# Performance work log

Hardware: AMD Instinct MI355X
Metric: run time of the kernel (lower is better)

## Reference

```python
import jax, jax.numpy as jnp
import numpy as np

N_NODES = 100000
N_EDGES = 1600000
FEAT = 128
BATCH = 2


def setup_inputs() -> dict:
    key = jax.random.key(0)
    ks = jax.random.split(key, 8)
    scale = 1.0 / np.sqrt(FEAT)
    return {
        "mesh_node_features": jax.random.normal(ks[0], (BATCH, N_NODES, FEAT), jnp.float32),
        "edge_index": jax.random.randint(ks[1], (N_EDGES, 2), 0, N_NODES, jnp.int64),
        "W1": jax.random.normal(ks[2], (FEAT, FEAT), jnp.float32) * scale,
        "b1": jnp.zeros((FEAT,), jnp.float32),
        "W2": jax.random.normal(ks[3], (FEAT, FEAT), jnp.float32) * scale,
        "b2": jnp.zeros((FEAT,), jnp.float32),
        "W3": jax.random.normal(ks[4], (FEAT, FEAT), jnp.float32) * scale,
        "b3": jnp.zeros((FEAT,), jnp.float32),
    }


def _gcn_layer(x, src, dst, norm, W, b, n_nodes):
    # x: [B, N, Fin] -> [B, N, Fout]; GCNConv: project, normalized scatter-sum, bias
    h = jnp.einsum("bnf,fg->bng", x, W)
    msg = h[:, src, :] * norm[None, :, None]          # [B, E+N, Fout]
    out = jnp.zeros_like(h).at[:, dst, :].add(msg)    # scatter over dst nodes
    return out + b


def reference(mesh_node_features, edge_index, W1, b1, W2, b2, W3, b3):
    n = mesh_node_features.shape[1]
    loops = jnp.arange(n, dtype=edge_index.dtype)
    src = jnp.concatenate([edge_index[:, 0], loops])  # self-loops appended
    dst = jnp.concatenate([edge_index[:, 1], loops])
    deg = jnp.zeros((n,), jnp.float32).at[dst].add(1.0)
    dinv = jax.lax.rsqrt(deg)                         # deg >= 1 due to self-loops
    norm = dinv[src] * dinv[dst]                      # symmetric GCN normalization

    x = mesh_node_features
    for W, b in ((W1, b1), (W2, b2), (W3, b3)):
        x = jax.nn.relu(_gcn_layer(x, src, dst, norm, W, b, n))
    return x
```

## Files before the change

### kernel.cpp

```cpp
#include <hip/hip_runtime.h>
#include <hip/hip_bf16.h>
#include <hip/hip_fp16.h>

#ifndef MINi
#define MINi(a,b) ((a)<(b)?(a):(b))
#endif

typedef _Float16 f16x8 __attribute__((ext_vector_type(8)));
typedef _Float16 f16x4 __attribute__((ext_vector_type(4)));
typedef float    f32x4 __attribute__((ext_vector_type(4)));

__global__ __launch_bounds__(256)
void cvt_kernel(const float* __restrict__ in, _Float16* __restrict__ out, int n4)
{
    int i = blockIdx.x * 256 + threadIdx.x;
    if (i >= n4) return;
    float4 v = ((const float4*)in)[i];
    f16x4 st = {(_Float16)v.x, (_Float16)v.y, (_Float16)v.z, (_Float16)v.w};
    ((f16x4*)out)[i] = st;
}

__global__ __launch_bounds__(256)
void wt_kernel(const float* __restrict__ W, _Float16* __restrict__ Wt)
{
    int idx = blockIdx.x * 256 + threadIdx.x;
    int k = idx >> 7, col = idx & 127;
    Wt[col * 128 + k] = (_Float16)W[idx];
}

__global__ __launch_bounds__(256)
void deg_kernel(const int* __restrict__ ei, int* __restrict__ cnt, int nE)
{
    int e = blockIdx.x * 256 + threadIdx.x;
    if (e >= nE) return;
    int2 p = ((const int2*)ei)[e];
    atomicAdd(&cnt[p.y], 1);
}

__global__ __launch_bounds__(256)
void scan_partials(const int* __restrict__ cnt, int* __restrict__ bsum, int n)
{
    __shared__ int red[4];
    int base = blockIdx.x * 1024;
    int t = threadIdx.x;
    int s = 0;
    #pragma unroll
    for (int i = 0; i < 4; ++i) {
        int idx = base + t * 4 + i;
        if (idx < n) s += cnt[idx];
    }
    #pragma unroll
    for (int off = 1; off < 64; off <<= 1) s += __shfl_xor(s, off);
    if ((t & 63) == 0) red[t >> 6] = s;
    __syncthreads();
    if (t == 0) bsum[blockIdx.x] = red[0] + red[1] + red[2] + red[3];
}

__global__ __launch_bounds__(128)
void scan_bsums(int* __restrict__ bsum, int nb)
{
    __shared__ int lds[128];
    int t = threadIdx.x;
    int v = (t < nb) ? bsum[t] : 0;
    lds[t] = v;
    __syncthreads();
    for (int off = 1; off < 128; off <<= 1) {
        int add = (t >= off) ? lds[t - off] : 0;
        __syncthreads();
        lds[t] += add;
        __syncthreads();
    }
    if (t < nb) bsum[t] = lds[t] - v;
}

__global__ __launch_bounds__(256)
void scan_final(const int* __restrict__ cnt, const int* __restrict__ bsum,
                int* __restrict__ row_start, int* __restrict__ cursor,
                float* __restrict__ dinv, int n, int nE)
{
    __shared__ int tsum[256];
    int base = blockIdx.x * 1024;
    int t = threadIdx.x;
    int c[4]; int s = 0;
    #pragma unroll
    for (int i = 0; i < 4; ++i) {
        int idx = base + t * 4 + i;
        c[i] = (idx < n) ? cnt[idx] : 0;
        s += c[i];
    }
    tsum[t] = s;
    __syncthreads();
    for (int off = 1; off < 256; off <<= 1) {
        int add = (t >= off) ? tsum[t - off] : 0;
        __syncthreads();
        tsum[t] += add;
        __syncthreads();
    }
    int run = bsum[blockIdx.x] + tsum[t] - s;
    #pragma unroll
    for (int i = 0; i < 4; ++i) {
        int idx = base + t * 4 + i;
        if (idx < n) {
            row_start[idx] = run;
            cursor[idx]    = run;
            dinv[idx]      = rsqrtf((float)(c[i] + 1));
            run += c[i];
        }
    }
    if (blockIdx.x == 0 && t == 0) row_start[n] = nE;
}

__global__ __launch_bounds__(256)
void fill_kernel(const int* __restrict__ ei, const float* __restrict__ dinv,
                 int* __restrict__ cursor, int2* __restrict__ csr, int nE)
{
    int e = blockIdx.x * 256 + threadIdx.x;
    if (e >= nE) return;
    int2 p = ((const int2*)ei)[e];
    int pos = atomicAdd(&cursor[p.y], 1);
    float nw = dinv[p.x] * dinv[p.y];
    csr[pos] = make_int2(p.x, __float_as_int(nw));
}

__global__ __launch_bounds__(256)
void agg_kernel(const _Float16* __restrict__ x, _Float16* __restrict__ out,
                const int* __restrict__ row_start, const int2* __restrict__ csr,
                const float* __restrict__ dinv, int n)
{
    int d = (blockIdx.x << 2) + (threadIdx.x >> 6);
    if (d >= n) return;
    int lane = threadIdx.x & 63;
    int hb   = lane >> 5;
    int fo   = (lane & 31) << 2;
    const _Float16* xb = x + (size_t)hb * n * 128 + fo;

    float sd = dinv[d], s2 = sd * sd;
    f16x4 xs = *(const f16x4*)(xb + (size_t)d * 128);
    float a0 = s2 * (float)xs[0], a1 = s2 * (float)xs[1];
    float a2 = s2 * (float)xs[2], a3 = s2 * (float)xs[3];

    int rs = row_start[d], re = row_start[d + 1];
    for (int e = rs; e < re; e += 64) {
        int idx = e + lane;
        int2 pk = csr[idx < re ? idx : re - 1];
        int cnt = MINi(re - e, 64);
        #pragma unroll 4
        for (int i = 0; i < cnt; ++i) {
            int   src = __shfl(pk.x, i);
            float nw  = __shfl(__int_as_float(pk.y), i);
            f16x4 rv = *(const f16x4*)(xb + (size_t)src * 128);
            a0 += nw * (float)rv[0]; a1 += nw * (float)rv[1];
            a2 += nw * (float)rv[2]; a3 += nw * (float)rv[3];
        }
    }
    f16x4 st = {(_Float16)a0, (_Float16)a1, (_Float16)a2, (_Float16)a3};
    *(f16x4*)(out + (size_t)(hb * n + d) * 128 + fo) = st;
}

template<bool HALF_OUT>
__global__ __launch_bounds__(256)
void gemm_mfma(const _Float16* __restrict__ A, const _Float16* __restrict__ Wt,
               const float* __restrict__ bias, void* __restrict__ outp, int nrows)
{
    int t  = threadIdx.x;
    int wv = t >> 6;
    int l  = t & 63;
    int lr = l & 15;
    int lk = l >> 4;
    size_t r0 = (size_t)blockIdx.x * 64;
    int c0 = wv * 32;

    f16x8 bf[2][4];
    #pragma unroll
    for (int ct = 0; ct < 2; ++ct)
        #pragma unroll
        for (int ks = 0; ks < 4; ++ks)
            bf[ct][ks] = *(const f16x8*)(Wt + (c0 + ct * 16 + lr) * 128 + ks * 32 + lk * 8);

    f32x4 acc[4][2];
    #pragma unroll
    for (int rt = 0; rt < 4; ++rt) {
        acc[rt][0] = (f32x4){0.f, 0.f, 0.f, 0.f};
        acc[rt][1] = (f32x4){0.f, 0.f, 0.f, 0.f};
    }

    #pragma unroll
    for (int rt = 0; rt < 4; ++rt) {
        #pragma unroll
        for (int ks = 0; ks < 4; ++ks) {
            f16x8 af = *(const f16x8*)(A + (r0 + rt * 16 + lr) * 128 + ks * 32 + lk * 8);
            acc[rt][0] = __builtin_amdgcn_mfma_f32_16x16x32_f16(af, bf[0][ks], acc[rt][0], 0, 0, 0);
            acc[rt][1] = __builtin_amdgcn_mfma_f32_16x16x32_f16(af, bf[1][ks], acc[rt][1], 0, 0, 0);
        }
    }

    float bc0 = bias[c0 + lr];
    float bc1 = bias[c0 + 16 + lr];
    #pragma unroll
    for (int rt = 0; rt < 4; ++rt) {
        #pragma unroll
        for (int ct = 0; ct < 2; ++ct) {
            float bc = ct ? bc1 : bc0;
            int col = c0 + ct * 16 + lr;
            #pragma unroll
            for (int r = 0; r < 4; ++r) {
                float v = fmaxf(acc[rt][ct][r] + bc, 0.f);
                size_t row = r0 + rt * 16 + lk * 4 + r;
                if constexpr (HALF_OUT)
                    ((_Float16*)outp)[row * 128 + col] = (_Float16)v;
                else
                    ((float*)outp)[row * 128 + col] = v;
            }
        }
    }
}

static inline size_t align_up(size_t x, size_t a) { return (x + a - 1) & ~(a - 1); }

extern "C" void kernel_launch(void* const* d_in, const int* in_sizes, int n_in,
                              void* d_out, int out_size, void* d_ws, size_t ws_size,
                              hipStream_t stream)
{
    const float* xin = (const float*)d_in[0];
    const int*   ei  = (const int*)d_in[1];
    const float* W1  = (const float*)d_in[2];
    const float* b1  = (const float*)d_in[3];
    const float* W2  = (const float*)d_in[4];
    const float* b2  = (const float*)d_in[5];
    const float* W3  = (const float*)d_in[6];
    const float* b3  = (const float*)d_in[7];
    float* out = (float*)d_out;

    const int N = in_sizes[0] / 256;
    const int E = in_sizes[1] / 2;
    const int ROWS = 2 * N;

    char* ws = (char*)d_ws;
    size_t off = 0;
    _Float16* Xh = (_Float16*)(ws + off);   off = align_up(off + (size_t)ROWS * 128 * 2, 256);
    _Float16* Ah = (_Float16*)(ws + off);   off = align_up(off + (size_t)ROWS * 128 * 2, 256);
    _Float16* Wt1 = (_Float16*)(ws + off);  off = align_up(off + 16384 * 2, 256);
    _Float16* Wt2 = (_Float16*)(ws + off);  off = align_up(off + 16384 * 2, 256);
    _Float16* Wt3 = (_Float16*)(ws + off);  off = align_up(off + 16384 * 2, 256);
    int* cnt = (int*)(ws + off);            off = align_up(off + (size_t)N * 4, 256);
    int* row_start = (int*)(ws + off);      off = align_up(off + (size_t)(N + 1) * 4, 256);
    int* cursor = (int*)(ws + off);         off = align_up(off + (size_t)N * 4, 256);
    float* dinvp = (float*)(ws + off);      off = align_up(off + (size_t)N * 4, 256);
    int* bsum = (int*)(ws + off);           off = align_up(off + 1024 * 4, 256);
    int2* csr = (int2*)(ws + off);          off = align_up(off + (size_t)E * 8, 256);

    const int nb = (N + 1023) / 1024;

    const int n4 = ROWS * 32;
    cvt_kernel<<<(n4 + 255) / 256, 256, 0, stream>>>(xin, Xh, n4);
    wt_kernel<<<64, 256, 0, stream>>>(W1, Wt1);
    wt_kernel<<<64, 256, 0, stream>>>(W2, Wt2);
    wt_kernel<<<64, 256, 0, stream>>>(W3, Wt3);

    hipMemsetAsync(cnt, 0, (size_t)N * 4, stream);
    deg_kernel<<<(E + 255) / 256, 256, 0, stream>>>(ei, cnt, E);
    scan_partials<<<nb, 256, 0, stream>>>(cnt, bsum, N);
    scan_bsums<<<1, 128, 0, stream>>>(bsum, nb);
    scan_final<<<nb, 256, 0, stream>>>(cnt, bsum, row_start, cursor, dinvp, N, E);
    fill_kernel<<<(E + 255) / 256, 256, 0, stream>>>(ei, dinvp, cursor, csr, E);

    const int agrid = (N + 3) / 4;
    const int ggrid = ROWS / 64;

    agg_kernel<<<agrid, 256, 0, stream>>>(Xh, Ah, row_start, csr, dinvp, N);
    gemm_mfma<true><<<ggrid, 256, 0, stream>>>(Ah, Wt1, b1, Xh, ROWS);
    agg_kernel<<<agrid, 256, 0, stream>>>(Xh, Ah, row_start, csr, dinvp, N);
    gemm_mfma<true><<<ggrid, 256, 0, stream>>>(Ah, Wt2, b2, Xh, ROWS);
    agg_kernel<<<agrid, 256, 0, stream>>>(Xh, Ah, row_start, csr, dinvp, N);
    gemm_mfma<false><<<ggrid, 256, 0, stream>>>(Ah, Wt3, b3, out, ROWS);
}
```

Measured before the change: 860.3 us.

## Fuse aggregation with MFMA GEMM per layer and single-pass decoupled scan

```diff
diff --git a/kernel.cpp b/kernel.cpp
--- a/kernel.cpp
+++ b/kernel.cpp
@@ -11,21 +11,34 @@
 typedef float    f32x4 __attribute__((ext_vector_type(4)));
 
 __global__ __launch_bounds__(256)
-void cvt_kernel(const float* __restrict__ in, _Float16* __restrict__ out, int n4)
-{
-    int i = blockIdx.x * 256 + threadIdx.x;
-    if (i >= n4) return;
-    float4 v = ((const float4*)in)[i];
-    f16x4 st = {(_Float16)v.x, (_Float16)v.y, (_Float16)v.z, (_Float16)v.w};
-    ((f16x4*)out)[i] = st;
-}
-
-__global__ __launch_bounds__(256)
-void wt_kernel(const float* __restrict__ W, _Float16* __restrict__ Wt)
-{
-    int idx = blockIdx.x * 256 + threadIdx.x;
-    int k = idx >> 7, col = idx & 127;
-    Wt[col * 128 + k] = (_Float16)W[idx];
+void prep_kernel(const float* __restrict__ xin, _Float16* __restrict__ Xh,
+                 const float* __restrict__ W1, const float* __restrict__ W2,
+                 const float* __restrict__ W3,
+                 _Float16* __restrict__ Wt1, _Float16* __restrict__ Wt2,
+                 _Float16* __restrict__ Wt3,
+                 int* __restrict__ zbase, int n4, int ncvt, int nzero)
+{
+    int b = blockIdx.x;
+    int t = threadIdx.x;
+    if (b < ncvt) {
+        int i = b * 256 + t;
+        if (i < n4) {
+            float4 v = ((const float4*)xin)[i];
+            f16x4 st = {(_Float16)v.x, (_Float16)v.y, (_Float16)v.z, (_Float16)v.w};
+            ((f16x4*)Xh)[i] = st;
+        }
+    } else if (b < ncvt + 192) {
+        int wb = b - ncvt;
+        int wi = wb >> 6;
+        int idx = (wb & 63) * 256 + t;
+        const float* W = (wi == 0) ? W1 : (wi == 1) ? W2 : W3;
+        _Float16* Wt = (wi == 0) ? Wt1 : (wi == 1) ? Wt2 : Wt3;
+        int k = idx >> 7, col = idx & 127;
+        Wt[col * 128 + k] = (_Float16)W[idx];
+    } else {
+        int i = (b - ncvt - 192) * 256 + t;
+        if (i < nzero) zbase[i] = 0;
+    }
 }
 
 __global__ __launch_bounds__(256)
@@ -37,50 +50,21 @@
     atomicAdd(&cnt[p.y], 1);
 }
 
-__global__ __launch_bounds__(256)
-void scan_partials(const int* __restrict__ cnt, int* __restrict__ bsum, int n)
-{
-    __shared__ int red[4];
-    int base = blockIdx.x * 1024;
+#define FLAG_AGG (1u << 30)
+#define FLAG_INC (2u << 30)
+#define VAL_MASK 0x3FFFFFFFu
+
+__global__ __launch_bounds__(256)
+void scan_kernel(const int* __restrict__ cnt, int* __restrict__ row_start,
+                 int* __restrict__ cursor, float* __restrict__ dinv,
+                 unsigned* __restrict__ status, int n, int nE)
+{
+    __shared__ int tsum[256];
+    __shared__ int sbase;
+    int b = blockIdx.x;
     int t = threadIdx.x;
-    int s = 0;
-    #pragma unroll
-    for (int i = 0; i < 4; ++i) {
-        int idx = base + t * 4 + i;
-        if (idx < n) s += cnt[idx];
-    }
-    #pragma unroll
-    for (int off = 1; off < 64; off <<= 1) s += __shfl_xor(s, off);
-    if ((t & 63) == 0) red[t >> 6] = s;
-    __syncthreads();
-    if (t == 0) bsum[blockIdx.x] = red[0] + red[1] + red[2] + red[3];
-}
-
-__global__ __launch_bounds__(128)
-void scan_bsums(int* __restrict__ bsum, int nb)
-{
-    __shared__ int lds[128];
-    int t = threadIdx.x;
-    int v = (t < nb) ? bsum[t] : 0;
-    lds[t] = v;
-    __syncthreads();
-    for (int off = 1; off < 128; off <<= 1) {
-        int add = (t >= off) ? lds[t - off] : 0;
-        __syncthreads();
-        lds[t] += add;
-        __syncthreads();
-    }
-    if (t < nb) bsum[t] = lds[t] - v;
-}
-
-__global__ __launch_bounds__(256)
-void scan_final(const int* __restrict__ cnt, const int* __restrict__ bsum,
-                int* __restrict__ row_start, int* __restrict__ cursor,
-                float* __restrict__ dinv, int n, int nE)
-{
-    __shared__ int tsum[256];
-    int base = blockIdx.x * 1024;
-    int t = threadIdx.x;
+    int base = b * 1024;
+
     int c[4]; int s = 0;
     #pragma unroll
     for (int i = 0; i < 4; ++i) {
@@ -96,7 +80,35 @@
         tsum[t] += add;
         __syncthreads();
     }
-    int run = bsum[blockIdx.x] + tsum[t] - s;
+
+    if (t == 0) {
+        int total = tsum[255];
+        if (b == 0) {
+            __hip_atomic_store(&status[0], FLAG_INC | (unsigned)total,
+                               __ATOMIC_RELAXED, __HIP_MEMORY_SCOPE_AGENT);
+            sbase = 0;
+        } else {
+            __hip_atomic_store(&status[b], FLAG_AGG | (unsigned)total,
+                               __ATOMIC_RELAXED, __HIP_MEMORY_SCOPE_AGENT);
+            int run = 0;
+            int j = b - 1;
+            while (true) {
+                unsigned w = __hip_atomic_load(&status[j], __ATOMIC_RELAXED,
+                                               __HIP_MEMORY_SCOPE_AGENT);
+                if (w == 0u) { __builtin_amdgcn_s_sleep(1); continue; }
+                run += (int)(w & VAL_MASK);
+                if (w & FLAG_INC) break;
+                --j;
+            }
+            int inc = run + total;
+            __hip_atomic_store(&status[b], FLAG_INC | (unsigned)inc,
+                               __ATOMIC_RELAXED, __HIP_MEMORY_SCOPE_AGENT);
+            sbase = inc - total;
+        }
+    }
+    __syncthreads();
+
+    int run = sbase + tsum[t] - s;
     #pragma unroll
     for (int i = 0; i < 4; ++i) {
         int idx = base + t * 4 + i;
@@ -107,7 +119,7 @@
             run += c[i];
         }
     }
-    if (blockIdx.x == 0 && t == 0) row_start[n] = nE;
+    if (b == 0 && t == 0) row_start[n] = nE;
 }
 
 __global__ __launch_bounds__(256)
@@ -122,95 +134,82 @@
     csr[pos] = make_int2(p.x, __float_as_int(nw));
 }
 
-__global__ __launch_bounds__(256)
-void agg_kernel(const _Float16* __restrict__ x, _Float16* __restrict__ out,
-                const int* __restrict__ row_start, const int2* __restrict__ csr,
-                const float* __restrict__ dinv, int n)
-{
-    int d = (blockIdx.x << 2) + (threadIdx.x >> 6);
-    if (d >= n) return;
-    int lane = threadIdx.x & 63;
+template<bool HALF_OUT>
+__global__ __launch_bounds__(256)
+void fused_kernel(const _Float16* __restrict__ x, void* __restrict__ outp,
+                  const _Float16* __restrict__ Wt, const float* __restrict__ bias,
+                  const int* __restrict__ row_start, const int2* __restrict__ csr,
+                  const float* __restrict__ dinv, int n)
+{
+    __shared__ _Float16 al[64][136];
+    int t    = threadIdx.x;
+    int wv   = t >> 6;
+    int lane = t & 63;
     int hb   = lane >> 5;
     int fo   = (lane & 31) << 2;
+    int d0   = blockIdx.x << 5;
     const _Float16* xb = x + (size_t)hb * n * 128 + fo;
 
-    float sd = dinv[d], s2 = sd * sd;
-    f16x4 xs = *(const f16x4*)(xb + (size_t)d * 128);
-    float a0 = s2 * (float)xs[0], a1 = s2 * (float)xs[1];
-    float a2 = s2 * (float)xs[2], a3 = s2 * (float)xs[3];
-
-    int rs = row_start[d], re = row_start[d + 1];
-    for (int e = rs; e < re; e += 64) {
-        int idx = e + lane;
-        int2 pk = csr[idx < re ? idx : re - 1];
-        int cnt = MINi(re - e, 64);
-        #pragma unroll 4
-        for (int i = 0; i < cnt; ++i) {
-            int   src = __shfl(pk.x, i);
-            float nw  = __shfl(__int_as_float(pk.y), i);
-            f16x4 rv = *(const f16x4*)(xb + (size_t)src * 128);
-            a0 += nw * (float)rv[0]; a1 += nw * (float)rv[1];
-            a2 += nw * (float)rv[2]; a3 += nw * (float)rv[3];
-        }
-    }
-    f16x4 st = {(_Float16)a0, (_Float16)a1, (_Float16)a2, (_Float16)a3};
-    *(f16x4*)(out + (size_t)(hb * n + d) * 128 + fo) = st;
-}
-
-template<bool HALF_OUT>
-__global__ __launch_bounds__(256)
-void gemm_mfma(const _Float16* __restrict__ A, const _Float16* __restrict__ Wt,
-               const float* __restrict__ bias, void* __restrict__ outp, int nrows)
-{
-    int t  = threadIdx.x;
-    int wv = t >> 6;
-    int l  = t & 63;
-    int lr = l & 15;
-    int lk = l >> 4;
-    size_t r0 = (size_t)blockIdx.x * 64;
-    int c0 = wv * 32;
-
-    f16x8 bf[2][4];
-    #pragma unroll
-    for (int ct = 0; ct < 2; ++ct)
+    for (int ni = 0; ni < 8; ++ni) {
+        int d = d0 + wv * 8 + ni;
+        float sd = dinv[d], s2 = sd * sd;
+        f16x4 xs = *(const f16x4*)(xb + (size_t)d * 128);
+        float a0 = s2 * (float)xs[0], a1 = s2 * (float)xs[1];
+        float a2 = s2 * (float)xs[2], a3 = s2 * (float)xs[3];
+
+        int rs = row_start[d], re = row_start[d + 1];
+        for (int e = rs; e < re; e += 64) {
+            int idx = e + lane;
+            int2 pk = csr[idx < re ? idx : re - 1];
+            int cntv = MINi(re - e, 64);
+            #pragma unroll 4
+            for (int i = 0; i < cntv; ++i) {
+                int   src = __shfl(pk.x, i);
+                float nw  = __shfl(__int_as_float(pk.y), i);
+                f16x4 rv = *(const f16x4*)(xb + (size_t)src * 128);
+                a0 += nw * (float)rv[0]; a1 += nw * (float)rv[1];
+                a2 += nw * (float)rv[2]; a3 += nw * (float)rv[3];
+            }
+        }
+        int lrow = hb * 32 + wv * 8 + ni;
+        f16x4 st = {(_Float16)a0, (_Float16)a1, (_Float16)a2, (_Float16)a3};
+        *(f16x4*)&al[lrow][fo] = st;
+    }
+    __syncthreads();
+
+    int lr = lane & 15;
+    int lk = lane >> 4;
+
+    f16x8 af[4];
+    #pragma unroll
+    for (int ks = 0; ks < 4; ++ks)
+        af[ks] = *(const f16x8*)&al[wv * 16 + lr][ks * 32 + lk * 8];
+
+    f32x4 acc[8];
+    #pragma unroll
+    for (int nt = 0; nt < 8; ++nt) acc[nt] = (f32x4){0.f, 0.f, 0.f, 0.f};
+
+    #pragma unroll
+    for (int ks = 0; ks < 4; ++ks) {
         #pragma unroll
-        for (int ks = 0; ks < 4; ++ks)
-            bf[ct][ks] = *(const f16x8*)(Wt + (c0 + ct * 16 + lr) * 128 + ks * 32 + lk * 8);
-
-    f32x4 acc[4][2];
-    #pragma unroll
-    for (int rt = 0; rt < 4; ++rt) {
-        acc[rt][0] = (f32x4){0.f, 0.f, 0.f, 0.f};
-        acc[rt][1] = (f32x4){0.f, 0.f, 0.f, 0.f};
-    }
-
-    #pragma unroll
-    for (int rt = 0; rt < 4; ++rt) {
+        for (int nt = 0; nt < 8; ++nt) {
+            f16x8 bf = *(const f16x8*)(Wt + (size_t)(nt * 16 + lr) * 128 + ks * 32 + lk * 8);
+            acc[nt] = __builtin_amdgcn_mfma_f32_16x16x32_f16(af[ks], bf, acc[nt], 0, 0, 0);
+        }
+    }
+
+    #pragma unroll
+    for (int nt = 0; nt < 8; ++nt) {
+        float bc = bias[nt * 16 + lr];
         #pragma unroll
-        for (int ks = 0; ks < 4; ++ks) {
-            f16x8 af = *(const f16x8*)(A + (r0 + rt * 16 + lr) * 128 + ks * 32 + lk * 8);
-            acc[rt][0] = __builtin_amdgcn_mfma_f32_16x16x32_f16(af, bf[0][ks], acc[rt][0], 0, 0, 0);
-            acc[rt][1] = __builtin_amdgcn_mfma_f32_16x16x32_f16(af, bf[1][ks], acc[rt][1], 0, 0, 0);
-        }
-    }
-
-    float bc0 = bias[c0 + lr];
-    float bc1 = bias[c0 + 16 + lr];
-    #pragma unroll
-    for (int rt = 0; rt < 4; ++rt) {
-        #pragma unroll
-        for (int ct = 0; ct < 2; ++ct) {
-            float bc = ct ? bc1 : bc0;
-            int col = c0 + ct * 16 + lr;
-            #pragma unroll
-            for (int r = 0; r < 4; ++r) {
-                float v = fmaxf(acc[rt][ct][r] + bc, 0.f);
-                size_t row = r0 + rt * 16 + lk * 4 + r;
-                if constexpr (HALF_OUT)
-                    ((_Float16*)outp)[row * 128 + col] = (_Float16)v;
-                else
-                    ((float*)outp)[row * 128 + col] = v;
-            }
+        for (int r = 0; r < 4; ++r) {
+            float v = fmaxf(acc[nt][r] + bc, 0.f);
+            int lrow = wv * 16 + lk * 4 + r;
+            size_t grow = (size_t)(lrow >> 5) * n + d0 + (lrow & 31);
+            if constexpr (HALF_OUT)
+                ((_Float16*)outp)[grow * 128 + nt * 16 + lr] = (_Float16)v;
+            else
+                ((float*)outp)[grow * 128 + nt * 16 + lr] = v;
         }
     }
 }
@@ -234,43 +233,35 @@
     const int N = in_sizes[0] / 256;
     const int E = in_sizes[1] / 2;
     const int ROWS = 2 * N;
+    const int nb = (N + 1023) / 1024;
 
     char* ws = (char*)d_ws;
     size_t off = 0;
     _Float16* Xh = (_Float16*)(ws + off);   off = align_up(off + (size_t)ROWS * 128 * 2, 256);
-    _Float16* Ah = (_Float16*)(ws + off);   off = align_up(off + (size_t)ROWS * 128 * 2, 256);
+    _Float16* Xn = (_Float16*)(ws + off);   off = align_up(off + (size_t)ROWS * 128 * 2, 256);
     _Float16* Wt1 = (_Float16*)(ws + off);  off = align_up(off + 16384 * 2, 256);
     _Float16* Wt2 = (_Float16*)(ws + off);  off = align_up(off + 16384 * 2, 256);
     _Float16* Wt3 = (_Float16*)(ws + off);  off = align_up(off + 16384 * 2, 256);
-    int* cnt = (int*)(ws + off);            off = align_up(off + (size_t)N * 4, 256);
+    int* cnt = (int*)(ws + off);            off += (size_t)N * 4;
+    unsigned* status = (unsigned*)(ws + off); off = align_up(off + (size_t)nb * 4, 256);
     int* row_start = (int*)(ws + off);      off = align_up(off + (size_t)(N + 1) * 4, 256);
     int* cursor = (int*)(ws + off);         off = align_up(off + (size_t)N * 4, 256);
     float* dinvp = (float*)(ws + off);      off = align_up(off + (size_t)N * 4, 256);
-    int* bsum = (int*)(ws + off);           off = align_up(off + 1024 * 4, 256);
     int2* csr = (int2*)(ws + off);          off = align_up(off + (size_t)E * 8, 256);
 
-    const int nb = (N + 1023) / 1024;
-
     const int n4 = ROWS * 32;
-    cvt_kernel<<<(n4 + 255) / 256, 256, 0, stream>>>(xin, Xh, n4);
-    wt_kernel<<<64, 256, 0, stream>>>(W1, Wt1);
-    wt_kernel<<<64, 256, 0, stream>>>(W2, Wt2);
-    wt_kernel<<<64, 256, 0, stream>>>(W3, Wt3);
-
-    hipMemsetAsync(cnt, 0, (size_t)N * 4, stream);
+    const int ncvt = (n4 + 255) / 256;
+    const int nzero = N + nb;
+    const int nzb = (nzero + 255) / 256;
+    prep_kernel<<<ncvt + 192 + nzb, 256, 0, stream>>>(
+        xin, Xh, W1, W2, W3, Wt1, Wt2, Wt3, cnt, n4, ncvt, nzero);
+
     deg_kernel<<<(E + 255) / 256, 256, 0, stream>>>(ei, cnt, E);
-    scan_partials<<<nb, 256, 0, stream>>>(cnt, bsum, N);
-    scan_bsums<<<1, 128, 0, stream>>>(bsum, nb);
-    scan_final<<<nb, 256, 0, stream>>>(cnt, bsum, row_start, cursor, dinvp, N, E);
+    scan_kernel<<<nb, 256, 0, stream>>>(cnt, row_start, cursor, dinvp, status, N, E);
     fill_kernel<<<(E + 255) / 256, 256, 0, stream>>>(ei, dinvp, cursor, csr, E);
 
-    const int agrid = (N + 3) / 4;
-    const int ggrid = ROWS / 64;
-
-    agg_kernel<<<agrid, 256, 0, stream>>>(Xh, Ah, row_start, csr, dinvp, N);
-    gemm_mfma<true><<<ggrid, 256, 0, stream>>>(Ah, Wt1, b1, Xh, ROWS);
-    agg_kernel<<<agrid, 256, 0, stream>>>(Xh, Ah, row_start, csr, dinvp, N);
-    gemm_mfma<true><<<ggrid, 256, 0, stream>>>(Ah, Wt2, b2, Xh, ROWS);
-    agg_kernel<<<agrid, 256, 0, stream>>>(Xh, Ah, row_start, csr, dinvp, N);
-    gemm_mfma<false><<<ggrid, 256, 0, stream>>>(Ah, Wt3, b3, out, ROWS);
-}
+    const int fgrid = N / 32;
+    fused_kernel<true><<<fgrid, 256, 0, stream>>>(Xh, Xn, Wt1, b1, row_start, csr, dinvp, N);
+    fused_kernel<true><<<fgrid, 256, 0, stream>>>(Xn, Xh, Wt2, b2, row_start, csr, dinvp, N);
+    fused_kernel<false><<<fgrid, 256, 0, stream>>>(Xh, out, Wt3, b3, row_start, csr, dinvp, N);
+}
```

Measured after the change: 1.016 ms. 18.1% more time.
